# Kernel optimization log

Hardware: AMD Instinct MI355X
Metric: run time of the kernel (lower is better)

Reference implementation:

```python
import jax, jax.numpy as jnp
import numpy as np

TAU = 0.1
EPS_NORM = 1e-12  # torch F.normalize clamp
EPS_DEN = 1e-6


def setup_inputs() -> dict:
    key = jax.random.key(0)
    k1, k2, k3, k4 = jax.random.split(key, 4)
    B, C, H, W = 4, 128, 64, 64
    feat_A = jax.random.normal(k1, (B, C, H, W), dtype=jnp.float32)
    feat_B = jax.random.normal(k2, (B, C, H, W), dtype=jnp.float32)
    H_mat = jax.random.normal(k3, (B, 3, 3), dtype=jnp.float32)
    valid_mask = jax.random.uniform(k4, (B, H, W), dtype=jnp.float32)
    return {"feat_A": feat_A, "feat_B": feat_B, "H_mat": H_mat, "valid_mask": valid_mask}


def _l2_normalize(x, axis):
    n = jnp.sqrt(jnp.sum(x * x, axis=axis, keepdims=True))
    return x / jnp.maximum(n, EPS_NORM)


def reference(feat_A, feat_B, H_mat, valid_mask):
    B, C, H, W = feat_A.shape
    HW = H * W
    fA = _l2_normalize(feat_A.reshape(B, C, HW), axis=1)  # [B, C, HW]
    fB = _l2_normalize(feat_B.reshape(B, C, HW), axis=1)  # [B, C, HW]
    # sim[b, n, m] = <fA[:, :, n], fB[:, :, m]> / tau
    sim = jnp.einsum('bcn,bcm->bnm', fA, fB) / TAU  # [B, HW, HW]
    # torch CE with input [B, HW, HW], labels arange(HW): class axis is 1,
    # so logits for position k are the column sim[b, :, k], target = k.
    lse = jax.nn.logsumexp(sim, axis=1)               # [B, HW] (over class axis)
    diag = jnp.einsum('bkk->bk', sim)                 # sim[b, k, k]
    loss = lse - diag                                  # [B, HW], per-position CE
    mask_flat = valid_mask.reshape(B, HW)
    return (loss * mask_flat).sum() / (mask_flat.sum() + EPS_DEN)
```

## Files before the change

kernel.cpp:

```cpp
#include <hip/hip_runtime.h>
#include <math.h>

#define BB 4
#define CC 128
#define HW 4096
#define SCF 3.798282565f

typedef short short8 __attribute__((ext_vector_type(8)));
typedef float f32x4 __attribute__((ext_vector_type(4)));

static __device__ inline unsigned short f2bf(float f) {
  unsigned int u = __float_as_uint(f);
  u += 0x7fffu + ((u >> 16) & 1u);
  return (unsigned short)(u >> 16);
}

static __device__ inline float fast_exp2(float x) {
#if __has_builtin(__builtin_amdgcn_exp2f)
  return __builtin_amdgcn_exp2f(x);
#else
  return exp2f(x);
#endif
}

__global__ __launch_bounds__(256) void k_prep(const float* __restrict__ fA,
                                              const float* __restrict__ fB,
                                              unsigned short* __restrict__ fAn,
                                              unsigned short* __restrict__ fBn,
                                              float* __restrict__ diag,
                                              float* __restrict__ expsum,
                                              float* __restrict__ acc) {
  __shared__ float sA[32 * 129];
  __shared__ float sB[32 * 129];
  __shared__ float red[3 * 256];

  const int bid = blockIdx.x;
  const int b   = bid >> 7;
  const int n0  = (bid & 127) * 32;
  const int tid = threadIdx.x;
  const int cR  = tid >> 5;
  const int n   = tid & 31;

  if (bid == 0 && tid == 0) { acc[0] = 0.f; acc[1] = 0.f; ((unsigned*)acc)[2] = 0u; }

  const float* pa = fA + (size_t)b * CC * HW + n0 + n;
  const float* pb = fB + (size_t)b * CC * HW + n0 + n;

  float ssa = 0.f, ssb = 0.f, dot = 0.f;
  #pragma unroll
  for (int it = 0; it < 16; ++it) {
    int c = it * 8 + cR;
    float va = pa[(size_t)c * HW];
    float vb = pb[(size_t)c * HW];
    sA[n * 129 + c] = va;
    sB[n * 129 + c] = vb;
    ssa = fmaf(va, va, ssa);
    ssb = fmaf(vb, vb, ssb);
    dot = fmaf(va, vb, dot);
  }
  red[tid] = ssa; red[256 + tid] = ssb; red[512 + tid] = dot;
  __syncthreads();

  if (tid < 32) {
    float sa = 0.f, sb = 0.f, dt = 0.f;
    #pragma unroll
    for (int k = 0; k < 8; ++k) {
      sa += red[k * 32 + tid];
      sb += red[256 + k * 32 + tid];
      dt += red[512 + k * 32 + tid];
    }
    float ia = 1.f / fmaxf(sqrtf(sa), 1e-12f);
    float ib = 1.f / fmaxf(sqrtf(sb), 1e-12f);
    int gidx = b * HW + n0 + tid;
    diag[gidx]   = dt * ia * ib * 10.f;
    expsum[gidx] = 0.f;
    red[tid]      = ia * SCF;
    red[32 + tid] = ib * SCF;
  }
  __syncthreads();

  #pragma unroll
  for (int r = 0; r < 2; ++r) {
    int L  = r * 256 + tid;
    int nn = L >> 4;
    int q  = L & 15;
    int c0 = (q ^ (nn & 7)) * 8;
    size_t base = ((size_t)b * HW + n0 + nn) * 128 + q * 8;
    {
      float sc = red[nn];
      const float* s = &sA[nn * 129 + c0];
      uint4 v;
      v.x = f2bf(s[0]*sc) | ((unsigned)f2bf(s[1]*sc) << 16);
      v.y = f2bf(s[2]*sc) | ((unsigned)f2bf(s[3]*sc) << 16);
      v.z = f2bf(s[4]*sc) | ((unsigned)f2bf(s[5]*sc) << 16);
      v.w = f2bf(s[6]*sc) | ((unsigned)f2bf(s[7]*sc) << 16);
      *(uint4*)(fAn + base) = v;
    }
    {
      float sc = red[32 + nn];
      const float* s = &sB[nn * 129 + c0];
      uint4 v;
      v.x = f2bf(s[0]*sc) | ((unsigned)f2bf(s[1]*sc) << 16);
      v.y = f2bf(s[2]*sc) | ((unsigned)f2bf(s[3]*sc) << 16);
      v.z = f2bf(s[4]*sc) | ((unsigned)f2bf(s[5]*sc) << 16);
      v.w = f2bf(s[6]*sc) | ((unsigned)f2bf(s[7]*sc) << 16);
      *(uint4*)(fBn + base) = v;
    }
  }
}

__global__ __launch_bounds__(256, 2) void k_main(const unsigned short* __restrict__ fAn,
                                                 const unsigned short* __restrict__ fBn,
                                                 float* __restrict__ expsum) {
  __shared__ unsigned short sB[128 * 128];
  __shared__ unsigned short sA[128 * 128];

  const int bid = blockIdx.x;
  const int x   = bid & 7;
  const int t   = bid >> 3;
  const int b   = x & 3;
  const int nq  = (x >> 2) | ((t & 1) << 1);
  const int mt  = t >> 1;
  const int m0  = mt * 128;
  const int nbase = nq * 1024;
  const int tid = threadIdx.x;

  const unsigned short* gB = fBn + ((size_t)b * HW + m0) * 128;
  #pragma unroll
  for (int r = 0; r < 8; ++r) {
    int L = r * 256 + tid;
    __builtin_amdgcn_global_load_lds(
        (const __attribute__((address_space(1))) unsigned int*)(gB + (size_t)L * 8),
        (__attribute__((address_space(3))) unsigned int*)(sB + L * 8), 16, 0, 0);
  }

  const int wv   = tid >> 6;
  const int lane = tid & 63;
  const int ml   = lane & 15;
  const int g    = lane >> 4;
  const int wn   = (wv & 1) * 64;
  const int wm   = (wv >> 1) * 64;

  float colAcc[4] = {0.f, 0.f, 0.f, 0.f};

  for (int it = 0; it < 8; ++it) {
    __syncthreads();
    const unsigned short* gA = fAn + ((size_t)b * HW + nbase + it * 128) * 128;
    #pragma unroll
    for (int r = 0; r < 8; ++r) {
      int L = r * 256 + tid;
      __builtin_amdgcn_global_load_lds(
          (const __attribute__((address_space(1))) unsigned int*)(gA + (size_t)L * 8),
          (__attribute__((address_space(3))) unsigned int*)(sA + L * 8), 16, 0, 0);
    }
    __syncthreads();

    f32x4 acc[4][4] = {};
    #pragma unroll
    for (int kc = 0; kc < 4; ++kc) {
      short8 af[4], bf[4];
      int q = kc * 4 + g;
      #pragma unroll
      for (int s = 0; s < 4; ++s) {
        int na = wn + s * 16 + ml;
        af[s] = *(const short8*)(sA + na * 128 + ((q ^ (na & 7)) * 8));
        int nb = wm + s * 16 + ml;
        bf[s] = *(const short8*)(sB + nb * 128 + ((q ^ (nb & 7)) * 8));
      }
      #pragma unroll
      for (int i = 0; i < 4; ++i)
        #pragma unroll
        for (int j = 0; j < 4; ++j)
          acc[i][j] = __builtin_amdgcn_mfma_f32_16x16x32_bf16(af[i], bf[j], acc[i][j], 0, 0, 0);
    }
    #pragma unroll
    for (int j = 0; j < 4; ++j) {
      float e = 0.f;
      #pragma unroll
      for (int i = 0; i < 4; ++i)
        #pragma unroll
        for (int r = 0; r < 4; ++r)
          e += fast_exp2(acc[i][j][r]);
      colAcc[j] += e;
    }
  }

  #pragma unroll
  for (int j = 0; j < 4; ++j) {
    float e = colAcc[j];
    e += __shfl_xor(e, 16, 64);
    e += __shfl_xor(e, 32, 64);
    if (lane < 16)
      atomicAdd(&expsum[(size_t)b * HW + m0 + wm + j * 16 + lane], e);
  }
}

__global__ __launch_bounds__(256) void k_loss(const float* __restrict__ diag,
                                              const float* __restrict__ expsum,
                                              const float* __restrict__ mask,
                                              float* __restrict__ acc,
                                              float* __restrict__ out) {
  __shared__ float rn[4], rd[4];
  const int i = blockIdx.x * 256 + threadIdx.x;
  float lse = __logf(expsum[i]);
  float mv  = mask[i];
  float num = mv * (lse - diag[i]);
  #pragma unroll
  for (int off = 32; off; off >>= 1) {
    num += __shfl_down(num, off, 64);
    mv  += __shfl_down(mv,  off, 64);
  }
  const int lane = threadIdx.x & 63, wv = threadIdx.x >> 6;
  if (lane == 0) { rn[wv] = num; rd[wv] = mv; }
  __syncthreads();
  if (threadIdx.x == 0) {
    float n = rn[0] + rn[1] + rn[2] + rn[3];
    float d = rd[0] + rd[1] + rd[2] + rd[3];
    atomicAdd(&acc[0], n);
    atomicAdd(&acc[1], d);
    __threadfence();
    unsigned prev = atomicAdd((unsigned*)(acc + 2), 1u);
    if (prev == 63u) {
      float fn = atomicAdd(&acc[0], 0.f);
      float fd = atomicAdd(&acc[1], 0.f);
      out[0] = fn / (fd + 1e-6f);
    }
  }
}

extern "C" void kernel_launch(void* const* d_in, const int* in_sizes, int n_in,
                              void* d_out, int out_size, void* d_ws, size_t ws_size,
                              hipStream_t stream) {
  const float* feat_A = (const float*)d_in[0];
  const float* feat_B = (const float*)d_in[1];
  const float* vmask  = (const float*)d_in[3];

  unsigned short* fAn = (unsigned short*)d_ws;
  unsigned short* fBn = fAn + (size_t)BB * HW * CC;
  float* diag   = (float*)(fBn + (size_t)BB * HW * CC);
  float* expsum = diag + BB * HW;
  float* acc    = expsum + BB * HW;
  float* out    = (float*)d_out;

  k_prep<<<512, 256, 0, stream>>>(feat_A, feat_B, fAn, fBn, diag, expsum, acc);
  k_main<<<512, 256, 0, stream>>>(fAn, fBn, expsum);
  k_loss<<<64,  256, 0, stream>>>(diag, expsum, vmask, acc, out);
}
```

Before: 97.29 us.

## Double-buffer A tiles in LDS and keep B fragments in registers

The main GEMM-exp kernel now keeps the B tile's MFMA fragments in registers for the whole block, so LDS space is freed for a second A buffer. The next A tile is prefetched with global_load_lds while the current tile is consumed, which removes one barrier per iteration and overlaps loads with MFMA and exp work. The cost is 64 extra VGPRs for the B fragments, which may hurt occupancy under launch_bounds(256,2). It also relies on the async LDS loads having completed by the single end-of-iteration barrier.

```diff
diff --git a/kernel.cpp b/kernel.cpp
--- a/kernel.cpp
+++ b/kernel.cpp
@@ -112,8 +112,7 @@
 __global__ __launch_bounds__(256, 2) void k_main(const unsigned short* __restrict__ fAn,
                                                  const unsigned short* __restrict__ fBn,
                                                  float* __restrict__ expsum) {
-  __shared__ unsigned short sB[128 * 128];
-  __shared__ unsigned short sA[128 * 128];
+  __shared__ unsigned short sA[2][128 * 128];
 
   const int bid = blockIdx.x;
   const int x   = bid & 7;
@@ -125,15 +124,6 @@
   const int nbase = nq * 1024;
   const int tid = threadIdx.x;
 
-  const unsigned short* gB = fBn + ((size_t)b * HW + m0) * 128;
-  #pragma unroll
-  for (int r = 0; r < 8; ++r) {
-    int L = r * 256 + tid;
-    __builtin_amdgcn_global_load_lds(
-        (const __attribute__((address_space(1))) unsigned int*)(gB + (size_t)L * 8),
-        (__attribute__((address_space(3))) unsigned int*)(sB + L * 8), 16, 0, 0);
-  }
-
   const int wv   = tid >> 6;
   const int lane = tid & 63;
   const int ml   = lane & 15;
@@ -141,37 +131,64 @@
   const int wn   = (wv & 1) * 64;
   const int wm   = (wv >> 1) * 64;
 
+  const unsigned short* gB = fBn + ((size_t)b * HW + m0) * 128;
+  const unsigned short* gA0 = fAn + ((size_t)b * HW + nbase) * 128;
+  #pragma unroll
+  for (int r = 0; r < 8; ++r) {
+    int L = r * 256 + tid;
+    __builtin_amdgcn_global_load_lds(
+        (const __attribute__((address_space(1))) unsigned int*)(gB + (size_t)L * 8),
+        (__attribute__((address_space(3))) unsigned int*)(sA[1] + L * 8), 16, 0, 0);
+    __builtin_amdgcn_global_load_lds(
+        (const __attribute__((address_space(1))) unsigned int*)(gA0 + (size_t)L * 8),
+        (__attribute__((address_space(3))) unsigned int*)(sA[0] + L * 8), 16, 0, 0);
+  }
+  __syncthreads();
+
+  short8 bfr[4][4];
+  #pragma unroll
+  for (int kc = 0; kc < 4; ++kc) {
+    int q = kc * 4 + g;
+    #pragma unroll
+    for (int s = 0; s < 4; ++s) {
+      int nb = wm + s * 16 + ml;
+      bfr[kc][s] = *(const short8*)(sA[1] + nb * 128 + ((q ^ (nb & 7)) * 8));
+    }
+  }
+  __syncthreads();
+
   float colAcc[4] = {0.f, 0.f, 0.f, 0.f};
 
+  #pragma unroll 2
   for (int it = 0; it < 8; ++it) {
-    __syncthreads();
-    const unsigned short* gA = fAn + ((size_t)b * HW + nbase + it * 128) * 128;
-    #pragma unroll
-    for (int r = 0; r < 8; ++r) {
-      int L = r * 256 + tid;
-      __builtin_amdgcn_global_load_lds(
-          (const __attribute__((address_space(1))) unsigned int*)(gA + (size_t)L * 8),
-          (__attribute__((address_space(3))) unsigned int*)(sA + L * 8), 16, 0, 0);
-    }
-    __syncthreads();
-
+    if (it < 7) {
+      const unsigned short* gA = fAn + ((size_t)b * HW + nbase + (it + 1) * 128) * 128;
+      unsigned short* dst = sA[(it + 1) & 1];
+      #pragma unroll
+      for (int r = 0; r < 8; ++r) {
+        int L = r * 256 + tid;
+        __builtin_amdgcn_global_load_lds(
+            (const __attribute__((address_space(1))) unsigned int*)(gA + (size_t)L * 8),
+            (__attribute__((address_space(3))) unsigned int*)(dst + L * 8), 16, 0, 0);
+      }
+    }
+
+    const unsigned short* src = sA[it & 1];
     f32x4 acc[4][4] = {};
     #pragma unroll
     for (int kc = 0; kc < 4; ++kc) {
-      short8 af[4], bf[4];
+      short8 af[4];
       int q = kc * 4 + g;
       #pragma unroll
       for (int s = 0; s < 4; ++s) {
         int na = wn + s * 16 + ml;
-        af[s] = *(const short8*)(sA + na * 128 + ((q ^ (na & 7)) * 8));
-        int nb = wm + s * 16 + ml;
-        bf[s] = *(const short8*)(sB + nb * 128 + ((q ^ (nb & 7)) * 8));
+        af[s] = *(const short8*)(src + na * 128 + ((q ^ (na & 7)) * 8));
       }
       #pragma unroll
       for (int i = 0; i < 4; ++i)
         #pragma unroll
         for (int j = 0; j < 4; ++j)
-          acc[i][j] = __builtin_amdgcn_mfma_f32_16x16x32_bf16(af[i], bf[j], acc[i][j], 0, 0, 0);
+          acc[i][j] = __builtin_amdgcn_mfma_f32_16x16x32_bf16(af[i], bfr[kc][j], acc[i][j], 0, 0, 0);
     }
     #pragma unroll
     for (int j = 0; j < 4; ++j) {
@@ -183,6 +200,8 @@
           e += fast_exp2(acc[i][j][r]);
       colAcc[j] += e;
     }
+
+    __syncthreads();
   }
 
   #pragma unroll
```

Result: no change. 96.33 us (-1.0%).
